# Kernel tuning notes

Measured on AMD Instinct MI355X. Metric: run time of the kernel, lower is better.

Reference implementation:

```python
import jax, jax.numpy as jnp
import numpy as np

MARGIN = 0.2
EPS = 1e-6  # torch.pairwise_distance adds eps to the difference before the norm


def setup_inputs() -> dict:
    key = jax.random.key(0)
    k1, k2, k3 = jax.random.split(key, 3)
    B, D = 8192, 128
    emb1 = jax.random.normal(k1, (B, D), dtype=jnp.float32)
    emb2 = jax.random.normal(k2, (B, D), dtype=jnp.float32)
    target = jax.random.randint(k3, (B,), 0, 2, dtype=jnp.int64)
    return {"emb1": emb1, "emb2": emb2, "target": target}


def reference(emb1, emb2, target):
    B, D = emb1.shape
    # torch.pairwise_distance(a, b) = ||a - b + EPS||_2; expand the square:
    # |a-b+eps|^2 = |a|^2 + |b|^2 - 2 a.b + 2*eps*(sum(a)-sum(b)) + D*eps^2
    sq = (
        jnp.sum(emb1 * emb1, axis=-1)[:, None]
        + jnp.sum(emb2 * emb2, axis=-1)[None, :]
        - 2.0 * (emb1 @ emb2.T)
        + 2.0 * EPS * (jnp.sum(emb1, axis=-1)[:, None] - jnp.sum(emb2, axis=-1)[None, :])
        + D * EPS * EPS
    )
    dist = jnp.sqrt(jnp.maximum(sq, 0.0))  # [B, B]: dist[i, j] = ||emb1[i] - emb2[j] + eps||

    pos = target == 1
    neg = target == 0
    # hardest positive: max over columns j with target[j]==1; hardest negative: min over target[j]==0
    pos_max = jnp.max(jnp.where(pos[None, :], dist, -jnp.inf), axis=1)  # [B]
    neg_min = jnp.min(jnp.where(neg[None, :], dist, jnp.inf), axis=1)   # [B]
    per_anchor = jnp.maximum(pos_max - neg_min + MARGIN, 0.0)
    anchor_w = pos.astype(dist.dtype)
    # mean over anchors (rows i with target[i]==1)
    return jnp.sum(per_anchor * anchor_w) / jnp.sum(anchor_w)
```

## Files before the change

kernel.cpp:

```cpp
#include <hip/hip_runtime.h>
#include <hip/hip_bf16.h>
#include <math.h>


#define DDIM   128
#define SPLITS 8
#define MARGIN 0.2f
#define EPS    1e-6f
#define SENT   1e30f

typedef unsigned short ushort_t;
typedef __attribute__((ext_vector_type(8))) short short8;
typedef __attribute__((ext_vector_type(8))) unsigned short ushort8;
typedef __attribute__((ext_vector_type(4))) float f32x4;

__device__ __forceinline__ ushort_t f2bf(float f) {
    unsigned int u = __float_as_uint(f);
    u = (u + 0x7FFFu + ((u >> 16) & 1u)) >> 16;
    return (ushort_t)u;
}

__global__ void prep_kernel(const float* __restrict__ e1, const float* __restrict__ e2,
                            const int* __restrict__ target,
                            float* __restrict__ rowterm,
                            float* __restrict__ cpos, float* __restrict__ cneg, int B) {
    int w    = (blockIdx.x * blockDim.x + threadIdx.x) >> 6;
    int lane = threadIdx.x & 63;
    if (w >= 2 * B) return;
    bool first = (w < B);
    int r = first ? w : w - B;
    const float* src = (first ? e1 : e2) + (size_t)r * DDIM;
    float2 v = *(const float2*)(src + lane * 2);
    float s = v.x + v.y;
    float n = v.x * v.x + v.y * v.y;
    #pragma unroll
    for (int off = 32; off > 0; off >>= 1) {
        s += __shfl_down(s, off, 64);
        n += __shfl_down(n, off, 64);
    }
    if (lane == 0) {
        if (first) {
            rowterm[r] = n + 2.f * EPS * s + (float)DDIM * EPS * EPS;
        } else {
            float ct = n - 2.f * EPS * s;
            int tg = target[r];
            cpos[r] = (tg == 1) ? ct : -SENT;
            cneg[r] = (tg == 0) ? ct :  SENT;
        }
    }
}

__device__ __forceinline__ void stage_tile(const float* __restrict__ g,
                                           ushort_t* __restrict__ lds, int tid) {
    #pragma unroll
    for (int it = 0; it < 8; ++it) {
        int idx = it * 256 + tid;
        int r   = idx >> 4;
        int c8  = idx & 15;
        const float* src = g + (size_t)r * DDIM + c8 * 8;
        float4 v0 = *(const float4*)src;
        float4 v1 = *(const float4*)(src + 4);
        ushort8 o;
        o[0] = f2bf(v0.x); o[1] = f2bf(v0.y); o[2] = f2bf(v0.z); o[3] = f2bf(v0.w);
        o[4] = f2bf(v1.x); o[5] = f2bf(v1.y); o[6] = f2bf(v1.z); o[7] = f2bf(v1.w);
        *(ushort8*)(lds + r * DDIM + c8 * 8) = o;
    }
}

__global__ __launch_bounds__(256, 2)
void tile_kernel(const float* __restrict__ e1, const float* __restrict__ e2,
                 const float* __restrict__ cpos, const float* __restrict__ cneg,
                 float* __restrict__ pmp, float* __restrict__ nmp, int B) {
    __shared__ __align__(16) ushort_t As[128 * DDIM];
    __shared__ __align__(16) ushort_t Bs[128 * DDIM];

    const int tid = threadIdx.x;
    const int w   = tid >> 6;
    const int l   = tid & 63;
    const int lq  = l >> 4;
    const int lm  = l & 15;
    const int row0 = blockIdx.x * 128;
    const int colSpan = B / SPLITS;
    const int col0 = blockIdx.y * colSpan;
    const int nTiles = colSpan / 128;

    stage_tile(e1 + (size_t)row0 * DDIM, As, tid);

    const int wr = (w >> 1) * 64;
    const int wc = (w & 1) * 64;

    float pm[4][4], nm[4][4];
    #pragma unroll
    for (int i = 0; i < 4; ++i)
        #pragma unroll
        for (int r = 0; r < 4; ++r) { pm[i][r] = -SENT; nm[i][r] = SENT; }

    const ushort_t* aBase = As + (wr + lm) * DDIM + lq * 8;
    const ushort_t* bBase = Bs + (wc + lm) * DDIM + lq * 8;

    for (int t = 0; t < nTiles; ++t) {
        if (t) __syncthreads();
        stage_tile(e2 + (size_t)(col0 + t * 128) * DDIM, Bs, tid);
        __syncthreads();

        f32x4 acc[4][4];
        #pragma unroll
        for (int i = 0; i < 4; ++i)
            #pragma unroll
            for (int j = 0; j < 4; ++j)
                acc[i][j] = (f32x4){0.f, 0.f, 0.f, 0.f};

        #pragma unroll
        for (int kk = 0; kk < DDIM; kk += 32) {
            short8 af[4], bf[4];
            #pragma unroll
            for (int i = 0; i < 4; ++i)
                af[i] = *(const short8*)(aBase + i * 16 * DDIM + kk);
            #pragma unroll
            for (int j = 0; j < 4; ++j)
                bf[j] = *(const short8*)(bBase + j * 16 * DDIM + kk);
            #pragma unroll
            for (int i = 0; i < 4; ++i)
                #pragma unroll
                for (int j = 0; j < 4; ++j)
                    acc[i][j] = __builtin_amdgcn_mfma_f32_16x16x32_bf16(
                                    af[i], bf[j], acc[i][j], 0, 0, 0);
        }

        #pragma unroll
        for (int j = 0; j < 4; ++j) {
            int col = col0 + t * 128 + wc + j * 16 + lm;
            float cp = cpos[col];
            float cn = cneg[col];
            #pragma unroll
            for (int i = 0; i < 4; ++i)
                #pragma unroll
                for (int r = 0; r < 4; ++r) {
                    float d = acc[i][j][r];
                    pm[i][r] = fmaxf(pm[i][r], fmaf(-2.f, d, cp));
                    nm[i][r] = fminf(nm[i][r], fmaf(-2.f, d, cn));
                }
        }
    }

    #pragma unroll
    for (int m = 1; m < 16; m <<= 1) {
        #pragma unroll
        for (int i = 0; i < 4; ++i)
            #pragma unroll
            for (int r = 0; r < 4; ++r) {
                pm[i][r] = fmaxf(pm[i][r], __shfl_xor(pm[i][r], m, 64));
                nm[i][r] = fminf(nm[i][r], __shfl_xor(nm[i][r], m, 64));
            }
    }

    __syncthreads();
    float* smP = (float*)As;
    float* smN = smP + 128;
    if ((w & 1) == 1 && lm == 0) {
        #pragma unroll
        for (int i = 0; i < 4; ++i)
            #pragma unroll
            for (int r = 0; r < 4; ++r) {
                int lr = wr + i * 16 + lq * 4 + r;
                smP[lr] = pm[i][r];
                smN[lr] = nm[i][r];
            }
    }
    __syncthreads();
    if ((w & 1) == 0 && lm == 0) {
        #pragma unroll
        for (int i = 0; i < 4; ++i)
            #pragma unroll
            for (int r = 0; r < 4; ++r) {
                int lr  = wr + i * 16 + lq * 4 + r;
                int row = row0 + lr;
                pmp[(size_t)blockIdx.y * B + row] = fmaxf(pm[i][r], smP[lr]);
                nmp[(size_t)blockIdx.y * B + row] = fminf(nm[i][r], smN[lr]);
            }
    }
}

__global__ void reduce_kernel(const float* __restrict__ pmp, const float* __restrict__ nmp,
                              const float* __restrict__ rowterm, const int* __restrict__ target,
                              float* __restrict__ bsum, float* __restrict__ bcnt, int B) {
    const int rowsPer = B / gridDim.x;
    const int base = blockIdx.x * rowsPer;
    float s = 0.f, c = 0.f;
    for (int i = threadIdx.x; i < rowsPer; i += blockDim.x) {
        int row = base + i;
        float pmv = -SENT, nmv = SENT;
        #pragma unroll
        for (int sp = 0; sp < SPLITS; ++sp) {
            pmv = fmaxf(pmv, pmp[(size_t)sp * B + row]);
            nmv = fminf(nmv, nmp[(size_t)sp * B + row]);
        }
        float rt = rowterm[row];
        float dp = sqrtf(fmaxf(rt + pmv, 0.f));
        float dn = sqrtf(fmaxf(rt + nmv, 0.f));
        if (target[row] == 1) {
            s += fmaxf(dp - dn + MARGIN, 0.f);
            c += 1.f;
        }
    }
    #pragma unroll
    for (int off = 32; off > 0; off >>= 1) {
        s += __shfl_down(s, off, 64);
        c += __shfl_down(c, off, 64);
    }
    __shared__ float ls[4], lc[4];
    int wv = threadIdx.x >> 6, ln = threadIdx.x & 63;
    if (ln == 0) { ls[wv] = s; lc[wv] = c; }
    __syncthreads();
    if (threadIdx.x == 0) {
        float ss = 0.f, cc = 0.f;
        #pragma unroll
        for (int i = 0; i < 4; ++i) { ss += ls[i]; cc += lc[i]; }
        bsum[blockIdx.x] = ss;
        bcnt[blockIdx.x] = cc;
    }
}

__global__ void final_kernel(const float* __restrict__ bsum, const float* __restrict__ bcnt,
                             float* __restrict__ out, int nb) {
    int lane = threadIdx.x;
    float s = (lane < nb) ? bsum[lane] : 0.f;
    float c = (lane < nb) ? bcnt[lane] : 0.f;
    #pragma unroll
    for (int off = 32; off > 0; off >>= 1) {
        s += __shfl_down(s, off, 64);
        c += __shfl_down(c, off, 64);
    }
    if (lane == 0) out[0] = s / c;
}

extern "C" void kernel_launch(void* const* d_in, const int* in_sizes, int n_in,
                              void* d_out, int out_size, void* d_ws, size_t ws_size,
                              hipStream_t stream) {
    const float* e1     = (const float*)d_in[0];
    const float* e2     = (const float*)d_in[1];
    const int*   target = (const int*)d_in[2];
    float* out = (float*)d_out;
    const int B = in_sizes[2];

    float* p = (float*)d_ws;
    float* rowterm = p;              p += B;
    float* cpos    = p;              p += B;
    float* cneg    = p;              p += B;
    float* pmp     = p;              p += (size_t)SPLITS * B;
    float* nmp     = p;              p += (size_t)SPLITS * B;
    float* bsum    = p;              p += 64;
    float* bcnt    = p;

    {
        int blocks = (2 * B + 3) / 4;
        prep_kernel<<<blocks, 256, 0, stream>>>(e1, e2, target, rowterm, cpos, cneg, B);
    }
    {
        dim3 grid(B / 128, SPLITS);
        tile_kernel<<<grid, 256, 0, stream>>>(e1, e2, cpos, cneg, pmp, nmp, B);
    }
    reduce_kernel<<<64, 256, 0, stream>>>(pmp, nmp, rowterm, target, bsum, bcnt, B);
    final_kernel<<<1, 64, 0, stream>>>(bsum, bcnt, out, 64);
}
```

Before: 111.9 us.

## XOR-swizzle LDS tiles for conflict-free MFMA loads and merge final reduction

Stores the bf16 tiles in LDS with a 16-byte chunk index XORed by the row index, and reads them back with the matching swizzled offset. This is meant to remove bank conflicts on the short8 fragment loads feeding the MFMAs. It also replaces the two-stage reduce and final kernels with a single 1024-thread block that writes the mean directly. That saves one kernel launch but makes the reduction serial within one block.

Measured after the change: 99.32 us. 11.2% less time.

```diff
diff --git a/kernel.cpp b/kernel.cpp
--- a/kernel.cpp
+++ b/kernel.cpp
@@ -63,7 +63,8 @@
         ushort8 o;
         o[0] = f2bf(v0.x); o[1] = f2bf(v0.y); o[2] = f2bf(v0.z); o[3] = f2bf(v0.w);
         o[4] = f2bf(v1.x); o[5] = f2bf(v1.y); o[6] = f2bf(v1.z); o[7] = f2bf(v1.w);
-        *(ushort8*)(lds + r * DDIM + c8 * 8) = o;
+        int pos = c8 ^ (r & 15);
+        *(ushort8*)(lds + r * DDIM + pos * 8) = o;
     }
 }
 
@@ -95,8 +96,8 @@
         #pragma unroll
         for (int r = 0; r < 4; ++r) { pm[i][r] = -SENT; nm[i][r] = SENT; }
 
-    const ushort_t* aBase = As + (wr + lm) * DDIM + lq * 8;
-    const ushort_t* bBase = Bs + (wc + lm) * DDIM + lq * 8;
+    const ushort_t* aRow = As + (wr + lm) * DDIM;
+    const ushort_t* bRow = Bs + (wc + lm) * DDIM;
 
     for (int t = 0; t < nTiles; ++t) {
         if (t) __syncthreads();
@@ -112,13 +113,14 @@
 
         #pragma unroll
         for (int kk = 0; kk < DDIM; kk += 32) {
+            const int co = (((lq + (kk >> 3)) ^ lm) << 3);
             short8 af[4], bf[4];
             #pragma unroll
             for (int i = 0; i < 4; ++i)
-                af[i] = *(const short8*)(aBase + i * 16 * DDIM + kk);
+                af[i] = *(const short8*)(aRow + i * 16 * DDIM + co);
             #pragma unroll
             for (int j = 0; j < 4; ++j)
-                bf[j] = *(const short8*)(bBase + j * 16 * DDIM + kk);
+                bf[j] = *(const short8*)(bRow + j * 16 * DDIM + co);
             #pragma unroll
             for (int i = 0; i < 4; ++i)
                 #pragma unroll
@@ -183,12 +185,9 @@
 
 __global__ void reduce_kernel(const float* __restrict__ pmp, const float* __restrict__ nmp,
                               const float* __restrict__ rowterm, const int* __restrict__ target,
-                              float* __restrict__ bsum, float* __restrict__ bcnt, int B) {
-    const int rowsPer = B / gridDim.x;
-    const int base = blockIdx.x * rowsPer;
+                              float* __restrict__ out, int B) {
     float s = 0.f, c = 0.f;
-    for (int i = threadIdx.x; i < rowsPer; i += blockDim.x) {
-        int row = base + i;
+    for (int row = threadIdx.x; row < B; row += blockDim.x) {
         float pmv = -SENT, nmv = SENT;
         #pragma unroll
         for (int sp = 0; sp < SPLITS; ++sp) {
@@ -208,30 +207,16 @@
         s += __shfl_down(s, off, 64);
         c += __shfl_down(c, off, 64);
     }
-    __shared__ float ls[4], lc[4];
+    __shared__ float ls[16], lc[16];
     int wv = threadIdx.x >> 6, ln = threadIdx.x & 63;
     if (ln == 0) { ls[wv] = s; lc[wv] = c; }
     __syncthreads();
     if (threadIdx.x == 0) {
         float ss = 0.f, cc = 0.f;
-        #pragma unroll
-        for (int i = 0; i < 4; ++i) { ss += ls[i]; cc += lc[i]; }
-        bsum[blockIdx.x] = ss;
-        bcnt[blockIdx.x] = cc;
-    }
-}
-
-__global__ void final_kernel(const float* __restrict__ bsum, const float* __restrict__ bcnt,
-                             float* __restrict__ out, int nb) {
-    int lane = threadIdx.x;
-    float s = (lane < nb) ? bsum[lane] : 0.f;
-    float c = (lane < nb) ? bcnt[lane] : 0.f;
-    #pragma unroll
-    for (int off = 32; off > 0; off >>= 1) {
-        s += __shfl_down(s, off, 64);
-        c += __shfl_down(c, off, 64);
-    }
-    if (lane == 0) out[0] = s / c;
+        int nw = blockDim.x >> 6;
+        for (int i = 0; i < nw; ++i) { ss += ls[i]; cc += lc[i]; }
+        out[0] = ss / cc;
+    }
 }
 
 extern "C" void kernel_launch(void* const* d_in, const int* in_sizes, int n_in,
@@ -248,9 +233,7 @@
     float* cpos    = p;              p += B;
     float* cneg    = p;              p += B;
     float* pmp     = p;              p += (size_t)SPLITS * B;
-    float* nmp     = p;              p += (size_t)SPLITS * B;
-    float* bsum    = p;              p += 64;
-    float* bcnt    = p;
+    float* nmp     = p;
 
     {
         int blocks = (2 * B + 3) / 4;
@@ -260,6 +243,5 @@
         dim3 grid(B / 128, SPLITS);
         tile_kernel<<<grid, 256, 0, stream>>>(e1, e2, cpos, cneg, pmp, nmp, B);
     }
-    reduce_kernel<<<64, 256, 0, stream>>>(pmp, nmp, rowterm, target, bsum, bcnt, B);
-    final_kernel<<<1, 64, 0, stream>>>(bsum, bcnt, out, 64);
-}
+    reduce_kernel<<<1, 1024, 0, stream>>>(pmp, nmp, rowterm, target, out, B);
+}
```
